# Optimization experiments

Hardware: AMD Instinct MI355X
Metric: run time of the kernel (lower is better)

The kernel has to match this reference:

```python
import jax, jax.numpy as jnp
import numpy as np

N = 100000       # nodes
E = 1600000      # edges (avg degree 16)
IN_DIM = 64
HID_DIM = 128
OUT_DIM = 64

def setup_inputs() -> dict:
    key = jax.random.key(0)
    k = jax.random.split(key, 8)
    inp = jax.random.normal(k[0], (IN_DIM, N), dtype=jnp.float32)
    src = jax.random.randint(k[1], (E,), 0, N, dtype=jnp.int32)
    dst = jax.random.randint(k[2], (E,), 0, N, dtype=jnp.int32)
    # Linear params (torch nn.Linear: y = x @ W.T + b)
    s1 = 1.0 / np.sqrt(IN_DIM)
    W1 = jax.random.uniform(k[3], (HID_DIM, IN_DIM), jnp.float32, -s1, s1)
    b1 = jax.random.uniform(k[4], (HID_DIM,), jnp.float32, -s1, s1)
    s2 = 1.0 / np.sqrt(HID_DIM)
    W2 = jax.random.uniform(k[5], (OUT_DIM, HID_DIM), jnp.float32, -s2, s2)
    b2 = jax.random.uniform(k[6], (OUT_DIM,), jnp.float32, -s2, s2)
    return {"inp": inp, "src": src, "dst": dst, "W1": W1, "b1": b1, "W2": W2, "b2": b2}

def reference(inp, src, dst, W1, b1, W2, b2):
    # inp: [in_dim, N] (module passes transposed features)
    X = inp.T                                   # [N, in_dim] node features
    # update_all(copy_src, sum): gather src features, scatter-add at dst
    agg = jax.ops.segment_sum(X[src], dst, num_segments=X.shape[0])  # [N, in_dim]
    h = jax.nn.relu(agg @ W1.T + b1)            # [N, hidden]
    out = h @ W2.T + b2                         # [N, out_dim]
    return out.T                                 # [out_dim, N] (final .t())
```

## Files before the change

### kernel.cpp

```cpp
#include <hip/hip_runtime.h>
#include <hip/hip_bf16.h>
#include <stdint.h>

typedef unsigned short ushort_t;
using short8   = __attribute__((ext_vector_type(8))) short;
using float4v  = __attribute__((ext_vector_type(4))) float;
using uint4v   = __attribute__((ext_vector_type(4))) unsigned;

#define BSH    6
#define BUCKW  64
#define CAP    1536
#define NBMAX  2048
#define BINB   256
#define HPITCH 136
#define APITCH 36

__device__ __forceinline__ float bf2f(ushort_t u) {
    union { unsigned int i; float f; } v;
    v.i = ((unsigned int)u) << 16;
    return v.f;
}
__device__ __forceinline__ ushort_t f2b(float f) {
    union { float f; unsigned int i; } v;
    v.f = f;
    unsigned int u = v.i;
    unsigned int r = (u + 0x7fffu + ((u >> 16) & 1u)) >> 16;
    return (ushort_t)r;
}
__device__ __forceinline__ float blo2f(unsigned v) {
    union { unsigned i; float f; } u; u.i = v << 16; return u.f;
}
__device__ __forceinline__ float bhi2f(unsigned v) {
    union { unsigned i; float f; } u; u.i = v & 0xFFFF0000u; return u.f;
}

__global__ __launch_bounds__(1024) void prep_k(
        const float* __restrict__ inp, ushort_t* __restrict__ X, int N,
        const float* __restrict__ W1, const float* __restrict__ W2,
        ushort_t* __restrict__ w1b, ushort_t* __restrict__ w2b,
        const int* __restrict__ src, const int* __restrict__ dst,
        int* __restrict__ gcur, unsigned* __restrict__ bin, int E,
        int NB) {
    __shared__ int lcnt[NBMAX];
    __shared__ int gbase[NBMAX];
    __shared__ int lcur[NBMAX];
    int tid = threadIdx.x;

    if ((int)blockIdx.x >= BINB) {
        int tb = blockIdx.x - BINB;
        if (tb == 0) {
            for (int i = tid; i < 8192; i += 1024) {
                w1b[i] = f2b(W1[i]);
                w2b[i] = f2b(W2[i]);
            }
        }
        int db = tid >> 8;
        int nl = tid & 255;
        int nc = tb * 256 + nl;
        if (nc < N) {
            unsigned ib = (unsigned)(db * 16) * (unsigned)N + (unsigned)nc;
            float v[16];
#pragma unroll
            for (int r = 0; r < 16; ++r)
                v[r] = inp[ib + (unsigned)(r * N)];
            unsigned dw[8];
#pragma unroll
            for (int j = 0; j < 8; ++j)
                dw[j] = (unsigned)f2b(v[2 * j]) | ((unsigned)f2b(v[2 * j + 1]) << 16);
            unsigned* xp = (unsigned*)X + (((unsigned)nc) << 5) + (unsigned)(db << 3);
            uint4v a = {dw[0], dw[1], dw[2], dw[3]};
            uint4v b = {dw[4], dw[5], dw[6], dw[7]};
            *(uint4v*)(xp)     = a;
            *(uint4v*)(xp + 4) = b;
        }
    } else {
        int bid  = blockIdx.x;
        int Q    = (E + 3) >> 2;
        int chunk = (Q + BINB - 1) / BINB;
        int q0 = bid * chunk;
        int q1 = q0 + chunk;
        if (q1 > Q) q1 = Q;
        const int4* dst4 = (const int4*)dst;
        const int4* src4 = (const int4*)src;

        for (int b = tid; b < NB; b += 1024) lcnt[b] = 0;
        __syncthreads();

        for (int q = q0 + tid; q < q1; q += 1024) {
            int e = q << 2;
            if (e + 3 < E) {
                int4 d = dst4[q];
                atomicAdd(&lcnt[d.x >> BSH], 1);
                atomicAdd(&lcnt[d.y >> BSH], 1);
                atomicAdd(&lcnt[d.z >> BSH], 1);
                atomicAdd(&lcnt[d.w >> BSH], 1);
            } else {
                for (int k = e; k < E; ++k) atomicAdd(&lcnt[dst[k] >> BSH], 1);
            }
        }
        __syncthreads();

        for (int b = tid; b < NB; b += 1024) {
            int c = lcnt[b];
            gbase[b] = c ? atomicAdd(&gcur[b], c) : 0;
            lcur[b]  = 0;
        }
        __syncthreads();

        for (int q = q0 + tid; q < q1; q += 1024) {
            int e = q << 2;
            if (e + 3 < E) {
                int4 d = dst4[q];
                int4 s = src4[q];
                int dv[4] = {d.x, d.y, d.z, d.w};
                int sv[4] = {s.x, s.y, s.z, s.w};
#pragma unroll
                for (int k = 0; k < 4; ++k) {
                    int b   = dv[k] >> BSH;
                    int pos = gbase[b] + atomicAdd(&lcur[b], 1);
                    if (pos < CAP)
                        bin[(size_t)b * CAP + pos] =
                            ((unsigned)(dv[k] & (BUCKW - 1)) << 24) | (unsigned)sv[k];
                }
            } else {
                for (int k = e; k < E; ++k) {
                    int dv = dst[k];
                    int b  = dv >> BSH;
                    int pos = gbase[b] + atomicAdd(&lcur[b], 1);
                    if (pos < CAP)
                        bin[(size_t)b * CAP + pos] =
                            ((unsigned)(dv & (BUCKW - 1)) << 24) | (unsigned)src[k];
                }
            }
        }
    }
}

__global__ __launch_bounds__(256, 5) void bam_k(
        const unsigned* __restrict__ Xu, const unsigned* __restrict__ bin,
        const int* __restrict__ gcur,
        const ushort_t* __restrict__ W1, const float* __restrict__ b1,
        const ushort_t* __restrict__ W2, const float* __restrict__ b2,
        float* __restrict__ out, int N) {
    __shared__ unsigned agg_s[BUCKW * APITCH];
    __shared__ __align__(16) char pool[4 * 16 * HPITCH * 2];
    unsigned* sl  = (unsigned*)pool;
    int* ecnt = (int*)(pool + CAP * 4);
    int* sc   = ecnt + BUCKW;
    int* ecur = sc + BUCKW;

    int tid = threadIdx.x;
    int b   = blockIdx.x;

    int cnt = gcur[b];
    if (cnt > CAP) cnt = CAP;
    const unsigned* bb = bin + (size_t)b * CAP;

    if (tid < BUCKW) ecnt[tid] = 0;
    __syncthreads();

    for (int i = tid; i < cnt; i += 256)
        atomicAdd(&ecnt[bb[i] >> 24], 1);
    __syncthreads();

    if (tid < BUCKW) sc[tid] = ecnt[tid];
    __syncthreads();
#pragma unroll
    for (int off = 1; off < BUCKW; off <<= 1) {
        int v = 0;
        if (tid < BUCKW && tid >= off) v = sc[tid - off];
        __syncthreads();
        if (tid < BUCKW) sc[tid] += v;
        __syncthreads();
    }
    if (tid < BUCKW) { sc[tid] -= ecnt[tid]; ecur[tid] = 0; }
    __syncthreads();

    for (int i = tid; i < cnt; i += 256) {
        unsigned p = bb[i];
        int nl  = (int)(p >> 24);
        int pos = sc[nl] + atomicAdd(&ecur[nl], 1);
        sl[pos] = p;
    }
    __syncthreads();

    int wave = tid >> 6;
    int lane = tid & 63;
    int half = lane >> 5;
    unsigned cu = (unsigned)(lane & 31);

    for (int n = wave; n < BUCKW; n += 4) {
        int s0 = sc[n];
        int c  = ecnt[n];
        float alo0 = 0.f, ahi0 = 0.f, alo1 = 0.f, ahi1 = 0.f;
        int i = 0;
        for (; i + 16 <= c; i += 16) {
            unsigned p0 = sl[s0 + i +  0 + half], p1 = sl[s0 + i +  2 + half];
            unsigned p2 = sl[s0 + i +  4 + half], p3 = sl[s0 + i +  6 + half];
            unsigned p4 = sl[s0 + i +  8 + half], p5 = sl[s0 + i + 10 + half];
            unsigned p6 = sl[s0 + i + 12 + half], p7 = sl[s0 + i + 14 + half];
            unsigned v0 = Xu[((p0 & 0xFFFFFFu) << 5) | cu];
            unsigned v1 = Xu[((p1 & 0xFFFFFFu) << 5) | cu];
            unsigned v2 = Xu[((p2 & 0xFFFFFFu) << 5) | cu];
            unsigned v3 = Xu[((p3 & 0xFFFFFFu) << 5) | cu];
            unsigned v4 = Xu[((p4 & 0xFFFFFFu) << 5) | cu];
            unsigned v5 = Xu[((p5 & 0xFFFFFFu) << 5) | cu];
            unsigned v6 = Xu[((p6 & 0xFFFFFFu) << 5) | cu];
            unsigned v7 = Xu[((p7 & 0xFFFFFFu) << 5) | cu];
            alo0 += blo2f(v0); ahi0 += bhi2f(v0);
            alo1 += blo2f(v1); ahi1 += bhi2f(v1);
            alo0 += blo2f(v2); ahi0 += bhi2f(v2);
            alo1 += blo2f(v3); ahi1 += bhi2f(v3);
            alo0 += blo2f(v4); ahi0 += bhi2f(v4);
            alo1 += blo2f(v5); ahi1 += bhi2f(v5);
            alo0 += blo2f(v6); ahi0 += bhi2f(v6);
            alo1 += blo2f(v7); ahi1 += bhi2f(v7);
        }
        for (; i + 2 <= c; i += 2) {
            unsigned p = sl[s0 + i + half];
            unsigned v = Xu[((p & 0xFFFFFFu) << 5) | cu];
            alo0 += blo2f(v); ahi0 += bhi2f(v);
        }
        if (i + half < c) {
            unsigned p = sl[s0 + i + half];
            unsigned v = Xu[((p & 0xFFFFFFu) << 5) | cu];
            alo1 += blo2f(v); ahi1 += bhi2f(v);
        }
        float alo = alo0 + alo1;
        float ahi = ahi0 + ahi1;
        float blo = __shfl(alo, lane + 32);
        float bhi = __shfl(ahi, lane + 32);
        if (half == 0) {
            alo += blo; ahi += bhi;
            agg_s[n * APITCH + (int)cu] =
                (unsigned)f2b(alo) | ((unsigned)f2b(ahi) << 16);
        }
    }
    __syncthreads();

    ushort_t* hw = (ushort_t*)pool + (size_t)wave * (16 * HPITCH);
    int row  = lane & 15;
    int quad = lane >> 4;

    const unsigned* arow = agg_s + (wave * 16 + row) * APITCH;
    short8 a0 = *(const short8*)(arow + quad * 4);
    short8 a1 = *(const short8*)(arow + 16 + quad * 4);

    float4v zero = {0.f, 0.f, 0.f, 0.f};

#pragma unroll
    for (int g = 0; g < 2; ++g) {
        float4v acc[4];
#pragma unroll
        for (int nt = 0; nt < 4; ++nt) acc[nt] = zero;
#pragma unroll
        for (int nt = 0; nt < 4; ++nt) {
            const ushort_t* wp = W1 + (size_t)(g * 64 + nt * 16 + row) * 64 + quad * 8;
            short8 bf0 = *(const short8*)(wp);
            short8 bf1 = *(const short8*)(wp + 32);
            acc[nt] = __builtin_amdgcn_mfma_f32_16x16x32_bf16(a0, bf0, acc[nt], 0, 0, 0);
            acc[nt] = __builtin_amdgcn_mfma_f32_16x16x32_bf16(a1, bf1, acc[nt], 0, 0, 0);
        }
#pragma unroll
        for (int nt = 0; nt < 4; ++nt) {
            float bias = b1[g * 64 + nt * 16 + row];
#pragma unroll
            for (int r = 0; r < 4; ++r) {
                float v = acc[nt][r] + bias;
                v = v > 0.f ? v : 0.f;
                hw[(quad * 4 + r) * HPITCH + g * 64 + nt * 16 + row] = f2b(v);
            }
        }
    }
    __syncthreads();

    short8 a2[4];
#pragma unroll
    for (int kt = 0; kt < 4; ++kt)
        a2[kt] = *(const short8*)(hw + row * HPITCH + kt * 32 + quad * 8);

    float4v acc2[4];
#pragma unroll
    for (int nt = 0; nt < 4; ++nt) acc2[nt] = zero;

#pragma unroll
    for (int nt = 0; nt < 4; ++nt) {
#pragma unroll
        for (int kt = 0; kt < 4; ++kt) {
            short8 bfr = *(const short8*)(W2 + (size_t)(nt * 16 + row) * 128 +
                                          kt * 32 + quad * 8);
            acc2[nt] = __builtin_amdgcn_mfma_f32_16x16x32_bf16(a2[kt], bfr, acc2[nt], 0, 0, 0);
        }
    }

    int n0   = (b << BSH) + wave * 16;
    int node = n0 + quad * 4;
#pragma unroll
    for (int nt = 0; nt < 4; ++nt) {
        int ko = nt * 16 + row;
        float bias = b2[ko];
        float4v pk;
#pragma unroll
        for (int r = 0; r < 4; ++r) pk[r] = acc2[nt][r] + bias;
        if (node + 3 < N) {
            *(float4v*)(out + (size_t)ko * N + node) = pk;
        } else {
#pragma unroll
            for (int r = 0; r < 4; ++r)
                if (node + r < N) out[(size_t)ko * N + node + r] = pk[r];
        }
    }
}

__global__ __launch_bounds__(256) void bagg_k(
        const unsigned* __restrict__ Xu, const unsigned* __restrict__ bin,
        const int* __restrict__ gcur, unsigned* __restrict__ aggu, int N) {
    __shared__ unsigned sl[CAP];
    __shared__ int ecnt[BUCKW];
    __shared__ int sc[BUCKW];
    __shared__ int ecur[BUCKW];
    int tid = threadIdx.x;
    int b   = blockIdx.x;
    int lo  = b << BSH;

    int cnt = gcur[b];
    if (cnt > CAP) cnt = CAP;
    const unsigned* bb = bin + (size_t)b * CAP;

    if (tid < BUCKW) ecnt[tid] = 0;
    __syncthreads();
    for (int i = tid; i < cnt; i += 256)
        atomicAdd(&ecnt[bb[i] >> 24], 1);
    __syncthreads();
    if (tid < BUCKW) sc[tid] = ecnt[tid];
    __syncthreads();
#pragma unroll
    for (int off = 1; off < BUCKW; off <<= 1) {
        int v = 0;
        if (tid < BUCKW && tid >= off) v = sc[tid - off];
        __syncthreads();
        if (tid < BUCKW) sc[tid] += v;
        __syncthreads();
    }
    if (tid < BUCKW) { sc[tid] -= ecnt[tid]; ecur[tid] = 0; }
    __syncthreads();
    for (int i = tid; i < cnt; i += 256) {
        unsigned p = bb[i];
        int nl  = (int)(p >> 24);
        int pos = sc[nl] + atomicAdd(&ecur[nl], 1);
        sl[pos] = p;
    }
    __syncthreads();

    int wave = tid >> 6;
    int lane = tid & 63;
    int half = lane >> 5;
    unsigned cu = (unsigned)(lane & 31);

    for (int n = wave; n < BUCKW; n += 4) {
        int node = lo + n;
        if (node >= N) break;
        int s0 = sc[n];
        int c  = ecnt[n];
        float alo0 = 0.f, ahi0 = 0.f, alo1 = 0.f, ahi1 = 0.f;
        int i = 0;
        for (; i + 16 <= c; i += 16) {
            unsigned p0 = sl[s0 + i +  0 + half], p1 = sl[s0 + i +  2 + half];
            unsigned p2 = sl[s0 + i +  4 + half], p3 = sl[s0 + i +  6 + half];
            unsigned p4 = sl[s0 + i +  8 + half], p5 = sl[s0 + i + 10 + half];
            unsigned p6 = sl[s0 + i + 12 + half], p7 = sl[s0 + i + 14 + half];
            unsigned v0 = Xu[((p0 & 0xFFFFFFu) << 5) | cu];
            unsigned v1 = Xu[((p1 & 0xFFFFFFu) << 5) | cu];
            unsigned v2 = Xu[((p2 & 0xFFFFFFu) << 5) | cu];
            unsigned v3 = Xu[((p3 & 0xFFFFFFu) << 5) | cu];
            unsigned v4 = Xu[((p4 & 0xFFFFFFu) << 5) | cu];
            unsigned v5 = Xu[((p5 & 0xFFFFFFu) << 5) | cu];
            unsigned v6 = Xu[((p6 & 0xFFFFFFu) << 5) | cu];
            unsigned v7 = Xu[((p7 & 0xFFFFFFu) << 5) | cu];
            alo0 += blo2f(v0); ahi0 += bhi2f(v0);
            alo1 += blo2f(v1); ahi1 += bhi2f(v1);
            alo0 += blo2f(v2); ahi0 += bhi2f(v2);
            alo1 += blo2f(v3); ahi1 += bhi2f(v3);
            alo0 += blo2f(v4); ahi0 += bhi2f(v4);
            alo1 += blo2f(v5); ahi1 += bhi2f(v5);
            alo0 += blo2f(v6); ahi0 += bhi2f(v6);
            alo1 += blo2f(v7); ahi1 += bhi2f(v7);
        }
        for (; i + 2 <= c; i += 2) {
            unsigned p = sl[s0 + i + half];
            unsigned v = Xu[((p & 0xFFFFFFu) << 5) | cu];
            alo0 += blo2f(v); ahi0 += bhi2f(v);
        }
        if (i + half < c) {
            unsigned p = sl[s0 + i + half];
            unsigned v = Xu[((p & 0xFFFFFFu) << 5) | cu];
            alo1 += blo2f(v); ahi1 += bhi2f(v);
        }
        float alo = alo0 + alo1;
        float ahi = ahi0 + ahi1;
        float blo = __shfl(alo, lane + 32);
        float bhi = __shfl(ahi, lane + 32);
        if (half == 0) {
            alo += blo; ahi += bhi;
            aggu[(size_t)node * 32 + (int)cu] =
                (unsigned)f2b(alo) | ((unsigned)f2b(ahi) << 16);
        }
    }
}

__global__ __launch_bounds__(256) void mlp_k(
        const ushort_t* __restrict__ aggb,
        const ushort_t* __restrict__ W1, const float* __restrict__ b1,
        const ushort_t* __restrict__ W2, const float* __restrict__ b2,
        float* __restrict__ out, int N) {
    __shared__ ushort_t h_s[4][16 * HPITCH];

    int wave = threadIdx.x >> 6;
    int lane = threadIdx.x & 63;
    int row  = lane & 15;
    int quad = lane >> 4;
    int n0   = blockIdx.x * 64 + wave * 16;

    int anode = n0 + row;
    if (anode > N - 1) anode = N - 1;
    const ushort_t* ap = aggb + (size_t)anode * 64;
    short8 a0 = *(const short8*)(ap + quad * 8);
    short8 a1 = *(const short8*)(ap + 32 + quad * 8);

    float4v zero = {0.f, 0.f, 0.f, 0.f};
    float4v acc[8];
#pragma unroll
    for (int nt = 0; nt < 8; ++nt) acc[nt] = zero;

#pragma unroll
    for (int nt = 0; nt < 8; ++nt) {
        const ushort_t* wp = W1 + (size_t)(nt * 16 + row) * 64 + quad * 8;
        short8 bf0 = *(const short8*)(wp);
        short8 bf1 = *(const short8*)(wp + 32);
        acc[nt] = __builtin_amdgcn_mfma_f32_16x16x32_bf16(a0, bf0, acc[nt], 0, 0, 0);
        acc[nt] = __builtin_amdgcn_mfma_f32_16x16x32_bf16(a1, bf1, acc[nt], 0, 0, 0);
    }

    ushort_t* hw = h_s[wave];
#pragma unroll
    for (int nt = 0; nt < 8; ++nt) {
        float bias = b1[nt * 16 + row];
#pragma unroll
        for (int r = 0; r < 4; ++r) {
            float v = acc[nt][r] + bias;
            v = v > 0.f ? v : 0.f;
            hw[(quad * 4 + r) * HPITCH + nt * 16 + row] = f2b(v);
        }
    }
    __syncthreads();

    short8 a2[4];
#pragma unroll
    for (int kt = 0; kt < 4; ++kt)
        a2[kt] = *(const short8*)(hw + row * HPITCH + kt * 32 + quad * 8);

    float4v acc2[4];
#pragma unroll
    for (int nt = 0; nt < 4; ++nt) acc2[nt] = zero;

#pragma unroll
    for (int nt = 0; nt < 4; ++nt) {
#pragma unroll
        for (int kt = 0; kt < 4; ++kt) {
            short8 bfr = *(const short8*)(W2 + (size_t)(nt * 16 + row) * 128 +
                                          kt * 32 + quad * 8);
            acc2[nt] = __builtin_amdgcn_mfma_f32_16x16x32_bf16(a2[kt], bfr, acc2[nt], 0, 0, 0);
        }
    }

    int node = n0 + quad * 4;
    if (node < N) {
#pragma unroll
        for (int nt = 0; nt < 4; ++nt) {
            int ko = nt * 16 + row;
            float bias = b2[ko];
            float4v pk;
#pragma unroll
            for (int r = 0; r < 4; ++r) pk[r] = acc2[nt][r] + bias;
            *(float4v*)(out + (size_t)ko * N + node) = pk;
        }
    }
}

extern "C" void kernel_launch(void* const* d_in, const int* in_sizes, int n_in,
                              void* d_out, int out_size, void* d_ws, size_t ws_size,
                              hipStream_t stream) {
    const float* inp = (const float*)d_in[0];
    const int*   src = (const int*)d_in[1];
    const int*   dst = (const int*)d_in[2];
    const float* W1  = (const float*)d_in[3];
    const float* b1  = (const float*)d_in[4];
    const float* W2  = (const float*)d_in[5];
    const float* b2  = (const float*)d_in[6];
    float* out = (float*)d_out;

    int N  = in_sizes[0] / 64;
    int E  = in_sizes[1];
    int NB = (N + BUCKW - 1) >> BSH;

    size_t xBytes   = (size_t)N * 64 * 2;
    size_t binBytes = (size_t)NB * CAP * 4;
    size_t fusedNeed = xBytes + binBytes + 2 * 8192 * 2 + NBMAX * 4 + 256;

    int TB = (N + 255) / 256;

    if (ws_size >= fusedNeed) {
        char* w = (char*)d_ws;
        ushort_t* X    = (ushort_t*)w;
        unsigned* bin  = (unsigned*)(w + xBytes);
        ushort_t* w1b  = (ushort_t*)(w + xBytes + binBytes);
        ushort_t* w2b  = w1b + 8192;
        int*      gcur = (int*)(w2b + 8192);

        hipMemsetAsync(gcur, 0, NB * sizeof(int), stream);

        prep_k<<<BINB + TB, 1024, 0, stream>>>(inp, X, N, W1, W2, w1b, w2b,
                                               src, dst, gcur, bin, E, NB);

        bam_k<<<NB, 256, 0, stream>>>((const unsigned*)X, bin, gcur,
                                      w1b, b1, w2b, b2, out, N);
    } else {
        ushort_t* aggb = (ushort_t*)d_ws;
        ushort_t* w1b  = aggb + (size_t)N * 64;
        ushort_t* w2b  = w1b + 8192;
        int*      gcur = (int*)(w2b + 8192);

        char*     ob  = (char*)d_out;
        ushort_t* X   = (ushort_t*)ob;
        unsigned* bin = (unsigned*)(ob + xBytes);

        hipMemsetAsync(gcur, 0, NB * sizeof(int), stream);

        prep_k<<<BINB + TB, 1024, 0, stream>>>(inp, X, N, W1, W2, w1b, w2b,
                                               src, dst, gcur, bin, E, NB);

        bagg_k<<<NB, 256, 0, stream>>>((const unsigned*)X, bin, gcur,
                                       (unsigned*)aggb, N);

        int tb = (N + 63) / 64;
        mlp_k<<<tb, 256, 0, stream>>>(aggb, w1b, b1, w2b, b2, out, N);
    }
}
```

Before: 212.7 us.

## Fuse prep and bucket-aggregate-MLP into persistent kernel with grid barrier

Replaces the two-kernel sequence (binning/convert prep kernel, then per-bucket aggregate+MLP kernel) with one persistent kernel sized to occupancy. A quarter of the blocks bin edges while the rest convert features to bf16. A software grid barrier then separates the phases, after which blocks pull buckets dynamically via an atomic ticket. This removes a kernel launch boundary and the tail imbalance of the second launch, at the cost of a spin barrier, a smaller block size for binning (256 vs 1024 threads, more global atomics on gcur), and reliance on all blocks being co-resident.

```diff
diff --git a/kernel.cpp b/kernel.cpp
--- a/kernel.cpp
+++ b/kernel.cpp
@@ -15,11 +15,6 @@
 #define HPITCH 136
 #define APITCH 36
 
-__device__ __forceinline__ float bf2f(ushort_t u) {
-    union { unsigned int i; float f; } v;
-    v.i = ((unsigned int)u) << 16;
-    return v.f;
-}
 __device__ __forceinline__ ushort_t f2b(float f) {
     union { float f; unsigned int i; } v;
     v.f = f;
@@ -34,59 +29,60 @@
     union { unsigned i; float f; } u; u.i = v & 0xFFFF0000u; return u.f;
 }
 
-__global__ __launch_bounds__(1024) void prep_k(
+__device__ __forceinline__ void gbar(int* cnt, int* gen, int nb) {
+    __threadfence();
+    __syncthreads();
+    if (threadIdx.x == 0) {
+        int g = __hip_atomic_load(gen, __ATOMIC_ACQUIRE, __HIP_MEMORY_SCOPE_AGENT);
+        int a = __hip_atomic_fetch_add(cnt, 1, __ATOMIC_ACQ_REL, __HIP_MEMORY_SCOPE_AGENT);
+        if (a == nb - 1) {
+            __hip_atomic_store(cnt, 0, __ATOMIC_RELAXED, __HIP_MEMORY_SCOPE_AGENT);
+            __hip_atomic_fetch_add(gen, 1, __ATOMIC_RELEASE, __HIP_MEMORY_SCOPE_AGENT);
+        } else {
+            int spins = 0;
+            while (__hip_atomic_load(gen, __ATOMIC_ACQUIRE, __HIP_MEMORY_SCOPE_AGENT) == g) {
+                __builtin_amdgcn_s_sleep(8);
+                if (++spins > (1 << 22)) break;
+            }
+        }
+    }
+    __syncthreads();
+    __threadfence();
+}
+
+__global__ __launch_bounds__(256, 4) void mega_k(
         const float* __restrict__ inp, ushort_t* __restrict__ X, int N,
-        const float* __restrict__ W1, const float* __restrict__ W2,
+        const float* __restrict__ W1f, const float* __restrict__ W2f,
         ushort_t* __restrict__ w1b, ushort_t* __restrict__ w2b,
         const int* __restrict__ src, const int* __restrict__ dst,
         int* __restrict__ gcur, unsigned* __restrict__ bin, int E,
-        int NB) {
-    __shared__ int lcnt[NBMAX];
-    __shared__ int gbase[NBMAX];
-    __shared__ int lcur[NBMAX];
+        int NB, int TB, int BB, int* __restrict__ bar,
+        const float* __restrict__ b1, const float* __restrict__ b2,
+        float* __restrict__ out) {
+    __shared__ __align__(16) char P[26624];
+    __shared__ int bshare;
     int tid = threadIdx.x;
-
-    if ((int)blockIdx.x >= BINB) {
-        int tb = blockIdx.x - BINB;
-        if (tb == 0) {
-            for (int i = tid; i < 8192; i += 1024) {
-                w1b[i] = f2b(W1[i]);
-                w2b[i] = f2b(W2[i]);
-            }
-        }
-        int db = tid >> 8;
-        int nl = tid & 255;
-        int nc = tb * 256 + nl;
-        if (nc < N) {
-            unsigned ib = (unsigned)(db * 16) * (unsigned)N + (unsigned)nc;
-            float v[16];
-#pragma unroll
-            for (int r = 0; r < 16; ++r)
-                v[r] = inp[ib + (unsigned)(r * N)];
-            unsigned dw[8];
-#pragma unroll
-            for (int j = 0; j < 8; ++j)
-                dw[j] = (unsigned)f2b(v[2 * j]) | ((unsigned)f2b(v[2 * j + 1]) << 16);
-            unsigned* xp = (unsigned*)X + (((unsigned)nc) << 5) + (unsigned)(db << 3);
-            uint4v a = {dw[0], dw[1], dw[2], dw[3]};
-            uint4v b = {dw[4], dw[5], dw[6], dw[7]};
-            *(uint4v*)(xp)     = a;
-            *(uint4v*)(xp + 4) = b;
-        }
-    } else {
-        int bid  = blockIdx.x;
-        int Q    = (E + 3) >> 2;
-        int chunk = (Q + BINB - 1) / BINB;
+    int* cnt = bar;
+    int* gen = bar + 1;
+    int* tick = bar + 2;
+
+    if ((int)blockIdx.x < BB) {
+        int* lcnt  = (int*)P;
+        int* gbase = lcnt + NBMAX;
+        int* lcur  = gbase + NBMAX;
+        int bid   = blockIdx.x;
+        int Q     = (E + 3) >> 2;
+        int chunk = (Q + BB - 1) / BB;
         int q0 = bid * chunk;
         int q1 = q0 + chunk;
         if (q1 > Q) q1 = Q;
         const int4* dst4 = (const int4*)dst;
         const int4* src4 = (const int4*)src;
 
-        for (int b = tid; b < NB; b += 1024) lcnt[b] = 0;
-        __syncthreads();
-
-        for (int q = q0 + tid; q < q1; q += 1024) {
+        for (int b = tid; b < NB; b += 256) lcnt[b] = 0;
+        __syncthreads();
+
+        for (int q = q0 + tid; q < q1; q += 256) {
             int e = q << 2;
             if (e + 3 < E) {
                 int4 d = dst4[q];
@@ -100,14 +96,14 @@
         }
         __syncthreads();
 
-        for (int b = tid; b < NB; b += 1024) {
+        for (int b = tid; b < NB; b += 256) {
             int c = lcnt[b];
             gbase[b] = c ? atomicAdd(&gcur[b], c) : 0;
             lcur[b]  = 0;
         }
         __syncthreads();
 
-        for (int q = q0 + tid; q < q1; q += 1024) {
+        for (int q = q0 + tid; q < q1; q += 256) {
             int e = q << 2;
             if (e + 3 < E) {
                 int4 d = dst4[q];
@@ -133,181 +129,315 @@
                 }
             }
         }
-    }
-}
-
-__global__ __launch_bounds__(256, 5) void bam_k(
-        const unsigned* __restrict__ Xu, const unsigned* __restrict__ bin,
-        const int* __restrict__ gcur,
-        const ushort_t* __restrict__ W1, const float* __restrict__ b1,
-        const ushort_t* __restrict__ W2, const float* __restrict__ b2,
-        float* __restrict__ out, int N) {
-    __shared__ unsigned agg_s[BUCKW * APITCH];
-    __shared__ __align__(16) char pool[4 * 16 * HPITCH * 2];
+    } else {
+        if ((int)blockIdx.x == BB) {
+            for (int i = tid; i < 8192; i += 256) {
+                w1b[i] = f2b(W1f[i]);
+                w2b[i] = f2b(W2f[i]);
+            }
+        }
+        int stride = (int)gridDim.x - BB;
+        for (int t = (int)blockIdx.x - BB; t < TB; t += stride) {
+            int nc = t * 256 + tid;
+            if (nc < N) {
+#pragma unroll
+                for (int db = 0; db < 4; ++db) {
+                    unsigned ib = (unsigned)(db * 16) * (unsigned)N + (unsigned)nc;
+                    float v[16];
+#pragma unroll
+                    for (int r = 0; r < 16; ++r)
+                        v[r] = inp[ib + (unsigned)(r * N)];
+                    unsigned dw[8];
+#pragma unroll
+                    for (int j = 0; j < 8; ++j)
+                        dw[j] = (unsigned)f2b(v[2 * j]) |
+                                ((unsigned)f2b(v[2 * j + 1]) << 16);
+                    unsigned* xp = (unsigned*)X + (((unsigned)nc) << 5) + (unsigned)(db << 3);
+                    uint4v a = {dw[0], dw[1], dw[2], dw[3]};
+                    uint4v b = {dw[4], dw[5], dw[6], dw[7]};
+                    *(uint4v*)(xp)     = a;
+                    *(uint4v*)(xp + 4) = b;
+                }
+            }
+        }
+    }
+
+    gbar(cnt, gen, (int)gridDim.x);
+
+    const unsigned* Xu = (const unsigned*)X;
+    unsigned* agg_s = (unsigned*)P;
+    char*     pool  = P + BUCKW * APITCH * 4;
     unsigned* sl  = (unsigned*)pool;
     int* ecnt = (int*)(pool + CAP * 4);
     int* sc   = ecnt + BUCKW;
     int* ecur = sc + BUCKW;
 
-    int tid = threadIdx.x;
-    int b   = blockIdx.x;
-
-    int cnt = gcur[b];
-    if (cnt > CAP) cnt = CAP;
-    const unsigned* bb = bin + (size_t)b * CAP;
-
-    if (tid < BUCKW) ecnt[tid] = 0;
-    __syncthreads();
-
-    for (int i = tid; i < cnt; i += 256)
-        atomicAdd(&ecnt[bb[i] >> 24], 1);
-    __syncthreads();
-
-    if (tid < BUCKW) sc[tid] = ecnt[tid];
-    __syncthreads();
-#pragma unroll
-    for (int off = 1; off < BUCKW; off <<= 1) {
-        int v = 0;
-        if (tid < BUCKW && tid >= off) v = sc[tid - off];
-        __syncthreads();
-        if (tid < BUCKW) sc[tid] += v;
-        __syncthreads();
-    }
-    if (tid < BUCKW) { sc[tid] -= ecnt[tid]; ecur[tid] = 0; }
-    __syncthreads();
-
-    for (int i = tid; i < cnt; i += 256) {
-        unsigned p = bb[i];
-        int nl  = (int)(p >> 24);
-        int pos = sc[nl] + atomicAdd(&ecur[nl], 1);
-        sl[pos] = p;
-    }
-    __syncthreads();
-
     int wave = tid >> 6;
     int lane = tid & 63;
     int half = lane >> 5;
     unsigned cu = (unsigned)(lane & 31);
-
-    for (int n = wave; n < BUCKW; n += 4) {
-        int s0 = sc[n];
-        int c  = ecnt[n];
-        float alo0 = 0.f, ahi0 = 0.f, alo1 = 0.f, ahi1 = 0.f;
-        int i = 0;
-        for (; i + 16 <= c; i += 16) {
-            unsigned p0 = sl[s0 + i +  0 + half], p1 = sl[s0 + i +  2 + half];
-            unsigned p2 = sl[s0 + i +  4 + half], p3 = sl[s0 + i +  6 + half];
-            unsigned p4 = sl[s0 + i +  8 + half], p5 = sl[s0 + i + 10 + half];
-            unsigned p6 = sl[s0 + i + 12 + half], p7 = sl[s0 + i + 14 + half];
-            unsigned v0 = Xu[((p0 & 0xFFFFFFu) << 5) | cu];
-            unsigned v1 = Xu[((p1 & 0xFFFFFFu) << 5) | cu];
-            unsigned v2 = Xu[((p2 & 0xFFFFFFu) << 5) | cu];
-            unsigned v3 = Xu[((p3 & 0xFFFFFFu) << 5) | cu];
-            unsigned v4 = Xu[((p4 & 0xFFFFFFu) << 5) | cu];
-            unsigned v5 = Xu[((p5 & 0xFFFFFFu) << 5) | cu];
-            unsigned v6 = Xu[((p6 & 0xFFFFFFu) << 5) | cu];
-            unsigned v7 = Xu[((p7 & 0xFFFFFFu) << 5) | cu];
-            alo0 += blo2f(v0); ahi0 += bhi2f(v0);
-            alo1 += blo2f(v1); ahi1 += bhi2f(v1);
-            alo0 += blo2f(v2); ahi0 += bhi2f(v2);
-            alo1 += blo2f(v3); ahi1 += bhi2f(v3);
-            alo0 += blo2f(v4); ahi0 += bhi2f(v4);
-            alo1 += blo2f(v5); ahi1 += bhi2f(v5);
-            alo0 += blo2f(v6); ahi0 += bhi2f(v6);
-            alo1 += blo2f(v7); ahi1 += bhi2f(v7);
-        }
-        for (; i + 2 <= c; i += 2) {
-            unsigned p = sl[s0 + i + half];
-            unsigned v = Xu[((p & 0xFFFFFFu) << 5) | cu];
-            alo0 += blo2f(v); ahi0 += bhi2f(v);
-        }
-        if (i + half < c) {
-            unsigned p = sl[s0 + i + half];
-            unsigned v = Xu[((p & 0xFFFFFFu) << 5) | cu];
-            alo1 += blo2f(v); ahi1 += bhi2f(v);
-        }
-        float alo = alo0 + alo1;
-        float ahi = ahi0 + ahi1;
-        float blo = __shfl(alo, lane + 32);
-        float bhi = __shfl(ahi, lane + 32);
-        if (half == 0) {
-            alo += blo; ahi += bhi;
-            agg_s[n * APITCH + (int)cu] =
-                (unsigned)f2b(alo) | ((unsigned)f2b(ahi) << 16);
-        }
-    }
-    __syncthreads();
-
-    ushort_t* hw = (ushort_t*)pool + (size_t)wave * (16 * HPITCH);
     int row  = lane & 15;
     int quad = lane >> 4;
 
-    const unsigned* arow = agg_s + (wave * 16 + row) * APITCH;
-    short8 a0 = *(const short8*)(arow + quad * 4);
-    short8 a1 = *(const short8*)(arow + 16 + quad * 4);
-
-    float4v zero = {0.f, 0.f, 0.f, 0.f};
-
-#pragma unroll
-    for (int g = 0; g < 2; ++g) {
-        float4v acc[4];
-#pragma unroll
-        for (int nt = 0; nt < 4; ++nt) acc[nt] = zero;
+    for (;;) {
+        __syncthreads();
+        if (tid == 0) bshare = atomicAdd(tick, 1);
+        __syncthreads();
+        int b = bshare;
+        if (b >= NB) break;
+
+        int cnt2 = gcur[b];
+        if (cnt2 > CAP) cnt2 = CAP;
+        const unsigned* bb = bin + (size_t)b * CAP;
+
+        if (tid < BUCKW) ecnt[tid] = 0;
+        __syncthreads();
+
+        for (int i = tid; i < cnt2; i += 256)
+            atomicAdd(&ecnt[bb[i] >> 24], 1);
+        __syncthreads();
+
+        if (tid < BUCKW) sc[tid] = ecnt[tid];
+        __syncthreads();
+#pragma unroll
+        for (int off = 1; off < BUCKW; off <<= 1) {
+            int v = 0;
+            if (tid < BUCKW && tid >= off) v = sc[tid - off];
+            __syncthreads();
+            if (tid < BUCKW) sc[tid] += v;
+            __syncthreads();
+        }
+        if (tid < BUCKW) { sc[tid] -= ecnt[tid]; ecur[tid] = 0; }
+        __syncthreads();
+
+        for (int i = tid; i < cnt2; i += 256) {
+            unsigned p = bb[i];
+            int nl  = (int)(p >> 24);
+            int pos = sc[nl] + atomicAdd(&ecur[nl], 1);
+            sl[pos] = p;
+        }
+        __syncthreads();
+
+        for (int n = wave; n < BUCKW; n += 4) {
+            int s0 = sc[n];
+            int c  = ecnt[n];
+            float alo0 = 0.f, ahi0 = 0.f, alo1 = 0.f, ahi1 = 0.f;
+            int i = 0;
+            for (; i + 16 <= c; i += 16) {
+                unsigned p0 = sl[s0 + i +  0 + half], p1 = sl[s0 + i +  2 + half];
+                unsigned p2 = sl[s0 + i +  4 + half], p3 = sl[s0 + i +  6 + half];
+                unsigned p4 = sl[s0 + i +  8 + half], p5 = sl[s0 + i + 10 + half];
+                unsigned p6 = sl[s0 + i + 12 + half], p7 = sl[s0 + i + 14 + half];
+                unsigned v0 = Xu[((p0 & 0xFFFFFFu) << 5) | cu];
+                unsigned v1 = Xu[((p1 & 0xFFFFFFu) << 5) | cu];
+                unsigned v2 = Xu[((p2 & 0xFFFFFFu) << 5) | cu];
+                unsigned v3 = Xu[((p3 & 0xFFFFFFu) << 5) | cu];
+                unsigned v4 = Xu[((p4 & 0xFFFFFFu) << 5) | cu];
+                unsigned v5 = Xu[((p5 & 0xFFFFFFu) << 5) | cu];
+                unsigned v6 = Xu[((p6 & 0xFFFFFFu) << 5) | cu];
+                unsigned v7 = Xu[((p7 & 0xFFFFFFu) << 5) | cu];
+                alo0 += blo2f(v0); ahi0 += bhi2f(v0);
+                alo1 += blo2f(v1); ahi1 += bhi2f(v1);
+                alo0 += blo2f(v2); ahi0 += bhi2f(v2);
+                alo1 += blo2f(v3); ahi1 += bhi2f(v3);
+                alo0 += blo2f(v4); ahi0 += bhi2f(v4);
+                alo1 += blo2f(v5); ahi1 += bhi2f(v5);
+                alo0 += blo2f(v6); ahi0 += bhi2f(v6);
+                alo1 += blo2f(v7); ahi1 += bhi2f(v7);
+            }
+            for (; i + 2 <= c; i += 2) {
+                unsigned p = sl[s0 + i + half];
+                unsigned v = Xu[((p & 0xFFFFFFu) << 5) | cu];
+                alo0 += blo2f(v); ahi0 += bhi2f(v);
+            }
+            if (i + half < c) {
+                unsigned p = sl[s0 + i + half];
+                unsigned v = Xu[((p & 0xFFFFFFu) << 5) | cu];
+                alo1 += blo2f(v); ahi1 += bhi2f(v);
+            }
+            float alo = alo0 + alo1;
+            float ahi = ahi0 + ahi1;
+            float blo = __shfl(alo, lane + 32);
+            float bhi = __shfl(ahi, lane + 32);
+            if (half == 0) {
+                alo += blo; ahi += bhi;
+                agg_s[n * APITCH + (int)cu] =
+                    (unsigned)f2b(alo) | ((unsigned)f2b(ahi) << 16);
+            }
+        }
+        __syncthreads();
+
+        ushort_t* hw = (ushort_t*)pool + (size_t)wave * (16 * HPITCH);
+
+        const unsigned* arow = agg_s + (wave * 16 + row) * APITCH;
+        short8 a0 = *(const short8*)(arow + quad * 4);
+        short8 a1 = *(const short8*)(arow + 16 + quad * 4);
+
+        float4v zero = {0.f, 0.f, 0.f, 0.f};
+
+#pragma unroll
+        for (int g = 0; g < 2; ++g) {
+            float4v acc[4];
+#pragma unroll
+            for (int nt = 0; nt < 4; ++nt) acc[nt] = zero;
+#pragma unroll
+            for (int nt = 0; nt < 4; ++nt) {
+                const ushort_t* wp = w1b + (size_t)(g * 64 + nt * 16 + row) * 64 + quad * 8;
+                short8 bf0 = *(const short8*)(wp);
+                short8 bf1 = *(const short8*)(wp + 32);
+                acc[nt] = __builtin_amdgcn_mfma_f32_16x16x32_bf16(a0, bf0, acc[nt], 0, 0, 0);
+                acc[nt] = __builtin_amdgcn_mfma_f32_16x16x32_bf16(a1, bf1, acc[nt], 0, 0, 0);
+            }
+#pragma unroll
+            for (int nt = 0; nt < 4; ++nt) {
+                float bias = b1[g * 64 + nt * 16 + row];
+#pragma unroll
+                for (int r = 0; r < 4; ++r) {
+                    float v = acc[nt][r] + bias;
+                    v = v > 0.f ? v : 0.f;
+                    hw[(quad * 4 + r) * HPITCH + g * 64 + nt * 16 + row] = f2b(v);
+                }
+            }
+        }
+        __syncthreads();
+
+        short8 a2[4];
+#pragma unroll
+        for (int kt = 0; kt < 4; ++kt)
+            a2[kt] = *(const short8*)(hw + row * HPITCH + kt * 32 + quad * 8);
+
+        float4v acc2[4];
+#pragma unroll
+        for (int nt = 0; nt < 4; ++nt) acc2[nt] = zero;
+
 #pragma unroll
         for (int nt = 0; nt < 4; ++nt) {
-            const ushort_t* wp = W1 + (size_t)(g * 64 + nt * 16 + row) * 64 + quad * 8;
-            short8 bf0 = *(const short8*)(wp);
-            short8 bf1 = *(const short8*)(wp + 32);
-            acc[nt] = __builtin_amdgcn_mfma_f32_16x16x32_bf16(a0, bf0, acc[nt], 0, 0, 0);
-            acc[nt] = __builtin_amdgcn_mfma_f32_16x16x32_bf16(a1, bf1, acc[nt], 0, 0, 0);
-        }
+#pragma unroll
+            for (int kt = 0; kt < 4; ++kt) {
+                short8 bfr = *(const short8*)(w2b + (size_t)(nt * 16 + row) * 128 +
+                                              kt * 32 + quad * 8);
+                acc2[nt] = __builtin_amdgcn_mfma_f32_16x16x32_bf16(a2[kt], bfr, acc2[nt], 0, 0, 0);
+            }
+        }
+
+        int n0   = (b << BSH) + wave * 16;
+        int node = n0 + quad * 4;
 #pragma unroll
         for (int nt = 0; nt < 4; ++nt) {
-            float bias = b1[g * 64 + nt * 16 + row];
-#pragma unroll
-            for (int r = 0; r < 4; ++r) {
-                float v = acc[nt][r] + bias;
-                v = v > 0.f ? v : 0.f;
-                hw[(quad * 4 + r) * HPITCH + g * 64 + nt * 16 + row] = f2b(v);
-            }
-        }
-    }
-    __syncthreads();
-
-    short8 a2[4];
-#pragma unroll
-    for (int kt = 0; kt < 4; ++kt)
-        a2[kt] = *(const short8*)(hw + row * HPITCH + kt * 32 + quad * 8);
-
-    float4v acc2[4];
-#pragma unroll
-    for (int nt = 0; nt < 4; ++nt) acc2[nt] = zero;
-
-#pragma unroll
-    for (int nt = 0; nt < 4; ++nt) {
-#pragma unroll
-        for (int kt = 0; kt < 4; ++kt) {
-            short8 bfr = *(const short8*)(W2 + (size_t)(nt * 16 + row) * 128 +
-                                          kt * 32 + quad * 8);
-            acc2[nt] = __builtin_amdgcn_mfma_f32_16x16x32_bf16(a2[kt], bfr, acc2[nt], 0, 0, 0);
-        }
-    }
-
-    int n0   = (b << BSH) + wave * 16;
-    int node = n0 + quad * 4;
-#pragma unroll
-    for (int nt = 0; nt < 4; ++nt) {
-        int ko = nt * 16 + row;
-        float bias = b2[ko];
-        float4v pk;
-#pragma unroll
-        for (int r = 0; r < 4; ++r) pk[r] = acc2[nt][r] + bias;
-        if (node + 3 < N) {
-            *(float4v*)(out + (size_t)ko * N + node) = pk;
-        } else {
-#pragma unroll
-            for (int r = 0; r < 4; ++r)
-                if (node + r < N) out[(size_t)ko * N + node + r] = pk[r];
+            int ko = nt * 16 + row;
+            float bias = b2[ko];
+            float4v pk;
+#pragma unroll
+            for (int r = 0; r < 4; ++r) pk[r] = acc2[nt][r] + bias;
+            if (node + 3 < N) {
+                *(float4v*)(out + (size_t)ko * N + node) = pk;
+            } else {
+#pragma unroll
+                for (int r = 0; r < 4; ++r)
+                    if (node + r < N) out[(size_t)ko * N + node + r] = pk[r];
+            }
+        }
+    }
+}
+
+__global__ __launch_bounds__(1024) void prep_k(
+        const float* __restrict__ inp, ushort_t* __restrict__ X, int N,
+        const float* __restrict__ W1, const float* __restrict__ W2,
+        ushort_t* __restrict__ w1b, ushort_t* __restrict__ w2b,
+        const int* __restrict__ src, const int* __restrict__ dst,
+        int* __restrict__ gcur, unsigned* __restrict__ bin, int E,
+        int NB) {
+    __shared__ int lcnt[NBMAX];
+    __shared__ int gbase[NBMAX];
+    __shared__ int lcur[NBMAX];
+    int tid = threadIdx.x;
+
+    if ((int)blockIdx.x >= BINB) {
+        int tb = blockIdx.x - BINB;
+        if (tb == 0) {
+            for (int i = tid; i < 8192; i += 1024) {
+                w1b[i] = f2b(W1[i]);
+                w2b[i] = f2b(W2[i]);
+            }
+        }
+        int db = tid >> 8;
+        int nl = tid & 255;
+        int nc = tb * 256 + nl;
+        if (nc < N) {
+            unsigned ib = (unsigned)(db * 16) * (unsigned)N + (unsigned)nc;
+            float v[16];
+#pragma unroll
+            for (int r = 0; r < 16; ++r)
+                v[r] = inp[ib + (unsigned)(r * N)];
+            unsigned dw[8];
+#pragma unroll
+            for (int j = 0; j < 8; ++j)
+                dw[j] = (unsigned)f2b(v[2 * j]) | ((unsigned)f2b(v[2 * j + 1]) << 16);
+            unsigned* xp = (unsigned*)X + (((unsigned)nc) << 5) + (unsigned)(db << 3);
+            uint4v a = {dw[0], dw[1], dw[2], dw[3]};
+            uint4v b = {dw[4], dw[5], dw[6], dw[7]};
+            *(uint4v*)(xp)     = a;
+            *(uint4v*)(xp + 4) = b;
+        }
+    } else {
+        int bid  = blockIdx.x;
+        int Q    = (E + 3) >> 2;
+        int chunk = (Q + BINB - 1) / BINB;
+        int q0 = bid * chunk;
+        int q1 = q0 + chunk;
+        if (q1 > Q) q1 = Q;
+        const int4* dst4 = (const int4*)dst;
+        const int4* src4 = (const int4*)src;
+
+        for (int b = tid; b < NB; b += 1024) lcnt[b] = 0;
+        __syncthreads();
+
+        for (int q = q0 + tid; q < q1; q += 1024) {
+            int e = q << 2;
+            if (e + 3 < E) {
+                int4 d = dst4[q];
+                atomicAdd(&lcnt[d.x >> BSH], 1);
+                atomicAdd(&lcnt[d.y >> BSH], 1);
+                atomicAdd(&lcnt[d.z >> BSH], 1);
+                atomicAdd(&lcnt[d.w >> BSH], 1);
+            } else {
+                for (int k = e; k < E; ++k) atomicAdd(&lcnt[dst[k] >> BSH], 1);
+            }
+        }
+        __syncthreads();
+
+        for (int b = tid; b < NB; b += 1024) {
+            int c = lcnt[b];
+            gbase[b] = c ? atomicAdd(&gcur[b], c) : 0;
+            lcur[b]  = 0;
+        }
+        __syncthreads();
+
+        for (int q = q0 + tid; q < q1; q += 1024) {
+            int e = q << 2;
+            if (e + 3 < E) {
+                int4 d = dst4[q];
+                int4 s = src4[q];
+                int dv[4] = {d.x, d.y, d.z, d.w};
+                int sv[4] = {s.x, s.y, s.z, s.w};
+#pragma unroll
+                for (int k = 0; k < 4; ++k) {
+                    int b   = dv[k] >> BSH;
+                    int pos = gbase[b] + atomicAdd(&lcur[b], 1);
+                    if (pos < CAP)
+                        bin[(size_t)b * CAP + pos] =
+                            ((unsigned)(dv[k] & (BUCKW - 1)) << 24) | (unsigned)sv[k];
+                }
+            } else {
+                for (int k = e; k < E; ++k) {
+                    int dv = dst[k];
+                    int b  = dv >> BSH;
+                    int pos = gbase[b] + atomicAdd(&lcur[b], 1);
+                    if (pos < CAP)
+                        bin[(size_t)b * CAP + pos] =
+                            ((unsigned)(dv & (BUCKW - 1)) << 24) | (unsigned)src[k];
+                }
+            }
         }
     }
 }
@@ -502,28 +632,38 @@
     int N  = in_sizes[0] / 64;
     int E  = in_sizes[1];
     int NB = (N + BUCKW - 1) >> BSH;
-
-    size_t xBytes   = (size_t)N * 64 * 2;
-    size_t binBytes = (size_t)NB * CAP * 4;
-    size_t fusedNeed = xBytes + binBytes + 2 * 8192 * 2 + NBMAX * 4 + 256;
-
     int TB = (N + 255) / 256;
 
-    if (ws_size >= fusedNeed) {
+    size_t xBytes    = (size_t)N * 64 * 2;
+    size_t binBytes  = (size_t)NB * CAP * 4;
+    size_t fusedNeed = xBytes + binBytes + 2 * 8192 * 2 + (NBMAX + 8) * 4 + 64;
+
+    static int gridB = -2;
+    if (gridB == -2) {
+        int perCU = 0, nCU = 0;
+        hipDeviceProp_t props;
+        if (hipGetDeviceProperties(&props, 0) == hipSuccess) nCU = props.multiProcessorCount;
+        if (hipOccupancyMaxActiveBlocksPerMultiprocessor(&perCU, mega_k, 256, 0) != hipSuccess)
+            perCU = 0;
+        long cap = (long)perCU * (long)nCU;
+        gridB = (cap >= 512) ? (int)(cap < 1024 ? cap : 1024) : -1;
+    }
+
+    if (ws_size >= fusedNeed && gridB > 0) {
         char* w = (char*)d_ws;
         ushort_t* X    = (ushort_t*)w;
         unsigned* bin  = (unsigned*)(w + xBytes);
         ushort_t* w1b  = (ushort_t*)(w + xBytes + binBytes);
         ushort_t* w2b  = w1b + 8192;
         int*      gcur = (int*)(w2b + 8192);
-
-        hipMemsetAsync(gcur, 0, NB * sizeof(int), stream);
-
-        prep_k<<<BINB + TB, 1024, 0, stream>>>(inp, X, N, W1, W2, w1b, w2b,
-                                               src, dst, gcur, bin, E, NB);
-
-        bam_k<<<NB, 256, 0, stream>>>((const unsigned*)X, bin, gcur,
-                                      w1b, b1, w2b, b2, out, N);
+        int*      bar  = gcur + NBMAX;
+
+        hipMemsetAsync(gcur, 0, (NBMAX + 8) * sizeof(int), stream);
+
+        int BB = gridB / 4;
+        mega_k<<<gridB, 256, 0, stream>>>(inp, X, N, W1, W2, w1b, w2b,
+                                          src, dst, gcur, bin, E, NB, TB, BB,
+                                          bar, b1, b2, out);
     } else {
         ushort_t* aggb = (ushort_t*)d_ws;
         ushort_t* w1b  = aggb + (size_t)N * 64;
```

Measured after the change: 641.5 us. 3.02x slower.
